# Kernel optimization log

Hardware: AMD Instinct MI355X
Metric: run time of the kernel (lower is better)

Reference implementation:

```python
import jax, jax.numpy as jnp
import numpy as np

ENT_TYPES = 9
INNER_DIM = 64
BIG_NEG = 1e12


def _rope_tables(seq_len, dim, dtype):
    # sinusoidal_position_embedding: interleaved [sin, cos] of pos * 10000^(-2i/d)
    pos = jnp.arange(seq_len, dtype=jnp.float32)[:, None]            # [S,1]
    inv_freq = jnp.power(10000.0, -2.0 * jnp.arange(dim // 2, dtype=jnp.float32) / dim)
    ang = pos * inv_freq                                             # [S,D/2]
    emb = jnp.stack([jnp.sin(ang), jnp.cos(ang)], axis=-1).reshape(seq_len, dim)  # [S,D]
    cos_pos = jnp.repeat(emb[:, 1::2], 2, axis=-1).astype(dtype)     # [S,D]
    sin_pos = jnp.repeat(emb[:, ::2], 2, axis=-1).astype(dtype)      # [S,D]
    return cos_pos, sin_pos


def _rotate_half(x):
    # stack([-x[...,1::2], x[...,::2]], -1).reshape(x.shape)
    return jnp.stack([-x[..., 1::2], x[..., ::2]], axis=-1).reshape(x.shape)


def setup_inputs() -> dict:
    key = jax.random.key(0)
    k1, k2 = jax.random.split(key)
    B, S, H = 16, 512, 1024
    last_hidden_state = jax.random.normal(k1, (B, S, H), dtype=jnp.float32)
    padding_mask = jnp.ones((B, S), dtype=jnp.float32)
    W = jax.random.normal(k2, (H, ENT_TYPES * INNER_DIM * 2), dtype=jnp.float32) * (1.0 / np.sqrt(H))
    b = jnp.zeros((ENT_TYPES * INNER_DIM * 2,), dtype=jnp.float32)
    return {"last_hidden_state": last_hidden_state, "padding_mask": padding_mask, "W": W, "b": b}


def reference(last_hidden_state, padding_mask, W, b):
    B, S, _ = last_hidden_state.shape
    H, D = ENT_TYPES, INNER_DIM
    out = last_hidden_state @ W + b                 # [B,S,H*2D]
    out = out.reshape(B, S, H, 2 * D)
    qw, kw = out[..., :D], out[..., D:]             # [B,S,H,D]

    cos_pos, sin_pos = _rope_tables(S, D, qw.dtype)  # [S,D]
    cos_pos = cos_pos[None, :, None, :]
    sin_pos = sin_pos[None, :, None, :]
    qw = qw * cos_pos + _rotate_half(qw) * sin_pos
    kw = kw * cos_pos + _rotate_half(kw) * sin_pos

    logits = jnp.einsum('bmhd,bnhd->bhmn', qw, kw)   # [B,H,S,S]
    pad = padding_mask[:, None, None, :]             # mask over key dim
    logits = logits * pad - (1.0 - pad) * BIG_NEG
    tril = jnp.tril(jnp.ones((S, S), dtype=logits.dtype), -1)
    logits = logits - tril * BIG_NEG
    return logits / jnp.sqrt(jnp.asarray(D, dtype=logits.dtype))
```

## Files before the change

kernel.cpp:

```cpp
#include <hip/hip_runtime.h>

#define EN 9
#define DD 64
#define SS 512
#define HH 1024
#define NOUT 1152

typedef float f32x4 __attribute__((ext_vector_type(4)));

#define GPTR(p) ((const __attribute__((address_space(1))) void*)(p))
#define LPTR(p) ((__attribute__((address_space(3))) void*)(p))

__device__ inline int pk4_fp8(float a, float b, float c, float d) {
  int v = __builtin_amdgcn_cvt_pk_fp8_f32(a, b, 0, false);
  v = __builtin_amdgcn_cvt_pk_fp8_f32(c, d, v, true);
  return v;
}

__global__ __launch_bounds__(256) void prep_kernel(
    const float* __restrict__ W, const float* __restrict__ X,
    unsigned char* __restrict__ Wf8, unsigned char* __restrict__ Xf8,
    float* __restrict__ ctab, float* __restrict__ stab) {
  if (blockIdx.x < 288u) {
    __shared__ float t[64][65];
    const int k0 = (blockIdx.x / 18) * 64;
    const int n0 = (blockIdx.x % 18) * 64;
    const int r = threadIdx.x >> 6;
    const int c = threadIdx.x & 63;
#pragma unroll
    for (int i = 0; i < 16; ++i) {
      const int kk = (i << 2) + r;
      t[kk][c] = W[(size_t)(k0 + kk) * NOUT + n0 + c];
    }
    __syncthreads();
#pragma unroll
    for (int i = 0; i < 2; ++i) {
      const int p = (i << 8) + threadIdx.x;
      const int n = p >> 3, cc = p & 7;
      const int kk = cc << 3;
      const int lo = pk4_fp8(t[kk][n], t[kk + 1][n], t[kk + 2][n], t[kk + 3][n]);
      const int hi =
          pk4_fp8(t[kk + 4][n], t[kk + 5][n], t[kk + 6][n], t[kk + 7][n]);
      const int gn = n0 + n;
      int2 v;
      v.x = lo;
      v.y = hi;
      *(int2*)(Wf8 + ((size_t)(k0 >> 6) * NOUT + gn) * 64 +
               ((cc ^ (gn & 7)) << 3)) = v;
    }
  } else if (blockIdx.x < 304u) {
    const int bt = blockIdx.x - 288;
#pragma unroll
    for (int j = 0; j < 4; ++j) {
      const int id = bt * 1024 + j * 256 + threadIdx.x;
      const int s = id >> 5, i = id & 31;
      const float freq = expf(-(float)(2 * i) * (9.210340371976184f / 64.0f));
      const float ang = (float)s * freq;
      ctab[id] = cosf(ang);
      stab[id] = sinf(ang);
    }
  } else {
    const int bt = blockIdx.x - 304;
#pragma unroll
    for (int j = 0; j < 4; ++j) {
      const int C = bt * 1024 + (j << 8) + threadIdx.x;
      const int row = C >> 7, c = C & 127;
      const float4 v0 = *(const float4*)(X + (size_t)C * 8);
      const float4 v1 = *(const float4*)(X + (size_t)C * 8 + 4);
      int2 v;
      v.x = pk4_fp8(v0.x, v0.y, v0.z, v0.w);
      v.y = pk4_fp8(v1.x, v1.y, v1.z, v1.w);
      *(int2*)(Xf8 + ((size_t)(c >> 3) * 8192 + row) * 64 +
               (((c ^ row) & 7) << 3)) = v;
    }
  }
}

__global__ __launch_bounds__(256, 4) void proj_rope_kernel(
    const unsigned char* __restrict__ Xf8, const unsigned char* __restrict__ Wf8,
    const float* __restrict__ bias, const float* __restrict__ ctab,
    const float* __restrict__ stab, unsigned char* __restrict__ QK) {
  __shared__ __align__(16) unsigned char sm[32768];
  const int tid = threadIdx.x;
  const int lane = tid & 63;
  const int wid = tid >> 6;
  const int wr = wid >> 1, wc = wid & 1;
  const int f = blockIdx.x;
  const int wkr = (f & 7) * 72 + (f >> 3);
  const int m0 = (wkr / 9) << 7;
  const int n0 = (wkr % 9) << 7;

  f32x4 acc[4][4];
#pragma unroll
  for (int i = 0; i < 4; ++i)
#pragma unroll
    for (int j = 0; j < 4; ++j) acc[i][j] = (f32x4){0.f, 0.f, 0.f, 0.f};

#define STAGE(BUF, T)                                                        \
  {                                                                          \
    const unsigned char* srcA_ = Xf8 + (((size_t)(T)*8192 + m0) << 6);       \
    const unsigned char* srcB_ = Wf8 + (((size_t)(T)*NOUT + n0) << 6);       \
    unsigned char* dst_ = sm + (BUF)*16384;                                  \
    _Pragma("unroll") for (int it = 0; it < 2; ++it) {                       \
      const int off_ = ((it << 8) + tid) << 4;                               \
      const int ldo_ = (((it << 8) + (wid << 6)) << 4);                      \
      __builtin_amdgcn_global_load_lds(GPTR(srcA_ + off_), LPTR(dst_ + ldo_), \
                                       16, 0, 0);                            \
      __builtin_amdgcn_global_load_lds(GPTR(srcB_ + off_),                   \
                                       LPTR(dst_ + 8192 + ldo_), 16, 0, 0);  \
    }                                                                        \
  }

#define COMPUTE(BUF)                                                         \
  {                                                                          \
    const unsigned char* smc_ = sm + (BUF)*16384;                            \
    __builtin_amdgcn_s_setprio(1);                                           \
    _Pragma("unroll") for (int kb = 0; kb < 2; ++kb) {                       \
      long aL[4], bL[4];                                                     \
      const int c8 = (kb << 2) + (lane >> 4);                                \
      _Pragma("unroll") for (int i = 0; i < 4; ++i) {                        \
        const int ra = (wr << 6) + (i << 4) + (lane & 15);                   \
        aL[i] = *(const long*)(smc_ + (ra << 6) + (((c8 ^ ra) & 7) << 3));   \
        const int rb = (wc << 6) + (i << 4) + (lane & 15);                   \
        bL[i] = *(const long*)(smc_ + 8192 + (rb << 6) +                     \
                               (((c8 ^ rb) & 7) << 3));                      \
      }                                                                      \
      _Pragma("unroll") for (int mi = 0; mi < 4; ++mi)                       \
          _Pragma("unroll") for (int ni = 0; ni < 4; ++ni) acc[mi][ni] =     \
          __builtin_amdgcn_mfma_f32_16x16x32_fp8_fp8(aL[mi], bL[ni],         \
                                                     acc[mi][ni], 0, 0, 0);  \
    }                                                                        \
    __builtin_amdgcn_s_setprio(0);                                           \
  }

  STAGE(0, 0)
#pragma unroll 1
  for (int t = 0; t < 15; ++t) {
    STAGE((t + 1) & 1, t + 1)
    asm volatile("s_waitcnt vmcnt(4)" ::: "memory");
    __builtin_amdgcn_s_barrier();
    __builtin_amdgcn_sched_barrier(0);
    COMPUTE(t & 1)
    __builtin_amdgcn_sched_barrier(0);
    __builtin_amdgcn_s_barrier();
  }
  asm volatile("s_waitcnt vmcnt(0)" ::: "memory");
  __builtin_amdgcn_s_barrier();
  __builtin_amdgcn_sched_barrier(0);
  COMPUTE(1)

  __syncthreads();
  float* scr = (float*)sm;
  const int erow = tid >> 3;
  const int ec8 = (tid & 7) << 1;
#pragma unroll
  for (int mi = 0; mi < 4; ++mi) {
#pragma unroll
    for (int ni = 0; ni < 4; ++ni) {
      const int col = (wc << 6) + (ni << 4) + (lane & 15);
#pragma unroll
      for (int r = 0; r < 4; ++r) {
        const int row = (wr << 4) + ((lane >> 4) << 2) + r;
        scr[row * 132 + col] = acc[mi][ni][r];
      }
    }
    __syncthreads();
    const int m = m0 + ((erow >> 4) << 6) + (mi << 4) + (erow & 15);
    const int s = m & (SS - 1);
    const int bb = m >> 9;
#pragma unroll
    for (int sl = 0; sl < 2; ++sl) {
      const int c8 = ec8 + sl;
      const int ncol = c8 << 3;
      const int n = n0 + ncol;
      const int h = n >> 7;
      const int t = (n >> 6) & 1;
      const int d0 = n & 63;
      const float scale = (t == 0) ? 0.125f : 1.0f;
      const float4 va = *(const float4*)&scr[erow * 132 + ncol];
      const float4 vb = *(const float4*)&scr[erow * 132 + ncol + 4];
      const float4 bia = *(const float4*)&bias[n];
      const float4 bib = *(const float4*)&bias[n + 4];
      const float4 cs = *(const float4*)&ctab[(s << 5) + (d0 >> 1)];
      const float4 sn = *(const float4*)&stab[(s << 5) + (d0 >> 1)];
      const float e0 = va.x + bia.x, o0 = va.y + bia.y;
      const float e1 = va.z + bia.z, o1 = va.w + bia.w;
      const float e2 = vb.x + bib.x, o2 = vb.y + bib.y;
      const float e3 = vb.z + bib.z, o3 = vb.w + bib.w;
      int2 ov;
      ov.x = pk4_fp8((e0 * cs.x - o0 * sn.x) * scale,
                     (o0 * cs.x + e0 * sn.x) * scale,
                     (e1 * cs.y - o1 * sn.y) * scale,
                     (o1 * cs.y + e1 * sn.y) * scale);
      ov.y = pk4_fp8((e2 * cs.z - o2 * sn.z) * scale,
                     (o2 * cs.z + e2 * sn.z) * scale,
                     (e3 * cs.w - o3 * sn.w) * scale,
                     (o3 * cs.w + e3 * sn.w) * scale);
      const int cswz = (((d0 >> 3) ^ (s & 7)) << 3);
      *(int2*)(QK + (((size_t)(bb * EN + h) * 2 + t) * SS + s) * DD + cswz) =
          ov;
    }
    __syncthreads();
  }
}

__global__ __launch_bounds__(256, 4) void logits_kernel(
    const unsigned char* __restrict__ QK, const float* __restrict__ pmask,
    float* __restrict__ out) {
  __shared__ __align__(16) unsigned char sm[16384];
  const int tid = threadIdx.x;
  const int lane = tid & 63;
  const int wid = tid >> 6;
  const int wr = wid >> 1, wc = wid & 1;
  const int f = blockIdx.x;
  const int wkr = (f & 7) * 288 + (f >> 3);
  const int bh = wkr >> 4;
  const int bb = bh / EN;
  const int tm = (wkr >> 2) & 3, tn = wkr & 3;
  const int mq0 = tm << 7, nk0 = tn << 7;
  const unsigned char* Qb = QK + (size_t)bh * 2 * SS * DD;
  const unsigned char* Kb = Qb + SS * DD;

#pragma unroll
  for (int it = 0; it < 2; ++it) {
    const int u = (it << 8) + tid;
    const int r = u >> 2, g = u & 3;
    __builtin_amdgcn_global_load_lds(
        GPTR(Qb + (size_t)(mq0 + r) * DD + (g << 4)),
        LPTR(sm + (((it << 8) + (wid << 6)) << 4)), 16, 0, 0);
    __builtin_amdgcn_global_load_lds(
        GPTR(Kb + (size_t)(nk0 + r) * DD + (g << 4)),
        LPTR(sm + 8192 + (((it << 8) + (wid << 6)) << 4)), 16, 0, 0);
  }
  __syncthreads();

  f32x4 acc[4][4];
#pragma unroll
  for (int i = 0; i < 4; ++i)
#pragma unroll
    for (int j = 0; j < 4; ++j) acc[i][j] = (f32x4){0.f, 0.f, 0.f, 0.f};

#pragma unroll
  for (int kb = 0; kb < 2; ++kb) {
    long aL[4], bL[4];
    const int c8 = (kb << 2) + (lane >> 4);
#pragma unroll
    for (int i = 0; i < 4; ++i) {
      const int ra = (wr << 6) + (i << 4) + (lane & 15);
      aL[i] = *(const long*)(sm + (ra << 6) + (((c8 ^ ra) & 7) << 3));
      const int rb = (wc << 6) + (i << 4) + (lane & 15);
      bL[i] = *(const long*)(sm + 8192 + (rb << 6) + (((c8 ^ rb) & 7) << 3));
    }
#pragma unroll
    for (int mi = 0; mi < 4; ++mi)
#pragma unroll
      for (int ni = 0; ni < 4; ++ni)
        acc[mi][ni] = __builtin_amdgcn_mfma_f32_16x16x32_fp8_fp8(
            aL[mi], bL[ni], acc[mi][ni], 0, 0, 0);
  }

#pragma unroll
  for (int mi = 0; mi < 4; ++mi) {
#pragma unroll
    for (int ni = 0; ni < 4; ++ni) {
      const int n = nk0 + (wc << 6) + (ni << 4) + (lane & 15);
      const float pd = pmask[bb * SS + n];
      const float sub = (1.0f - pd) * 1.25e11f;
#pragma unroll
      for (int r = 0; r < 4; ++r) {
        const int m = mq0 + (wr << 6) + (mi << 4) + ((lane >> 4) << 2) + r;
        float v = acc[mi][ni][r] * pd - sub;
        if (m > n) v -= 1.25e11f;
        out[((size_t)bh * SS + m) * SS + n] = v;
      }
    }
  }
}

extern "C" void kernel_launch(void* const* d_in, const int* in_sizes, int n_in,
                              void* d_out, int out_size, void* d_ws,
                              size_t ws_size, hipStream_t stream) {
  const float* X = (const float*)d_in[0];
  const float* pm = (const float*)d_in[1];
  const float* W = (const float*)d_in[2];
  const float* bias = (const float*)d_in[3];
  float* out = (float*)d_out;
  unsigned char* ws = (unsigned char*)d_ws;
  unsigned char* QK = ws;
  unsigned char* Wf8 = ws + 9437184;
  float* ctab = (float*)(ws + 10616832);
  float* stab = (float*)(ws + 10682368);
  unsigned char* Xf8 = ws + 10747904;

  prep_kernel<<<dim3(1328), dim3(256), 0, stream>>>(W, X, Wf8, Xf8, ctab, stab);
  proj_rope_kernel<<<dim3(576), dim3(256), 0, stream>>>(Xf8, Wf8, bias, ctab,
                                                        stab, QK);
  logits_kernel<<<dim3(2304), dim3(256), 0, stream>>>(QK, pm, out);
}
```

Baseline: 62.23 us.

## Load GEMM fragments directly from global memory, bypassing LDS staging

Both the projection GEMM and the logits GEMM now read their FP8 MFMA fragments straight from global memory into registers instead of staging tiles in LDS through global_load_lds with a double-buffered pipeline and barriers. This removes the LDS traffic and the synchronisation. It also drops the occupancy hint from launch_bounds. Each wave now issues redundant 8-byte global loads, which rely on L1/L2 for reuse, and the explicit load/compute overlap is gone, leaving only unroll-by-2 for latency hiding.

```diff
diff --git a/kernel.cpp b/kernel.cpp
--- a/kernel.cpp
+++ b/kernel.cpp
@@ -7,9 +7,6 @@
 #define NOUT 1152
 
 typedef float f32x4 __attribute__((ext_vector_type(4)));
-
-#define GPTR(p) ((const __attribute__((address_space(1))) void*)(p))
-#define LPTR(p) ((__attribute__((address_space(3))) void*)(p))
 
 __device__ inline int pk4_fp8(float a, float b, float c, float d) {
   int v = __builtin_amdgcn_cvt_pk_fp8_f32(a, b, 0, false);
@@ -76,11 +73,11 @@
   }
 }
 
-__global__ __launch_bounds__(256, 4) void proj_rope_kernel(
+__global__ __launch_bounds__(256) void proj_rope_kernel(
     const unsigned char* __restrict__ Xf8, const unsigned char* __restrict__ Wf8,
     const float* __restrict__ bias, const float* __restrict__ ctab,
     const float* __restrict__ stab, unsigned char* __restrict__ QK) {
-  __shared__ __align__(16) unsigned char sm[32768];
+  __shared__ __align__(16) float scr[32 * 132];
   const int tid = threadIdx.x;
   const int lane = tid & 63;
   const int wid = tid >> 6;
@@ -96,61 +93,34 @@
 #pragma unroll
     for (int j = 0; j < 4; ++j) acc[i][j] = (f32x4){0.f, 0.f, 0.f, 0.f};
 
-#define STAGE(BUF, T)                                                        \
-  {                                                                          \
-    const unsigned char* srcA_ = Xf8 + (((size_t)(T)*8192 + m0) << 6);       \
-    const unsigned char* srcB_ = Wf8 + (((size_t)(T)*NOUT + n0) << 6);       \
-    unsigned char* dst_ = sm + (BUF)*16384;                                  \
-    _Pragma("unroll") for (int it = 0; it < 2; ++it) {                       \
-      const int off_ = ((it << 8) + tid) << 4;                               \
-      const int ldo_ = (((it << 8) + (wid << 6)) << 4);                      \
-      __builtin_amdgcn_global_load_lds(GPTR(srcA_ + off_), LPTR(dst_ + ldo_), \
-                                       16, 0, 0);                            \
-      __builtin_amdgcn_global_load_lds(GPTR(srcB_ + off_),                   \
-                                       LPTR(dst_ + 8192 + ldo_), 16, 0, 0);  \
-    }                                                                        \
-  }
-
-#define COMPUTE(BUF)                                                         \
-  {                                                                          \
-    const unsigned char* smc_ = sm + (BUF)*16384;                            \
-    __builtin_amdgcn_s_setprio(1);                                           \
-    _Pragma("unroll") for (int kb = 0; kb < 2; ++kb) {                       \
-      long aL[4], bL[4];                                                     \
-      const int c8 = (kb << 2) + (lane >> 4);                                \
-      _Pragma("unroll") for (int i = 0; i < 4; ++i) {                        \
-        const int ra = (wr << 6) + (i << 4) + (lane & 15);                   \
-        aL[i] = *(const long*)(smc_ + (ra << 6) + (((c8 ^ ra) & 7) << 3));   \
-        const int rb = (wc << 6) + (i << 4) + (lane & 15);                   \
-        bL[i] = *(const long*)(smc_ + 8192 + (rb << 6) +                     \
-                               (((c8 ^ rb) & 7) << 3));                      \
-      }                                                                      \
-      _Pragma("unroll") for (int mi = 0; mi < 4; ++mi)                       \
-          _Pragma("unroll") for (int ni = 0; ni < 4; ++ni) acc[mi][ni] =     \
-          __builtin_amdgcn_mfma_f32_16x16x32_fp8_fp8(aL[mi], bL[ni],         \
-                                                     acc[mi][ni], 0, 0, 0);  \
-    }                                                                        \
-    __builtin_amdgcn_s_setprio(0);                                           \
-  }
-
-  STAGE(0, 0)
-#pragma unroll 1
-  for (int t = 0; t < 15; ++t) {
-    STAGE((t + 1) & 1, t + 1)
-    asm volatile("s_waitcnt vmcnt(4)" ::: "memory");
-    __builtin_amdgcn_s_barrier();
-    __builtin_amdgcn_sched_barrier(0);
-    COMPUTE(t & 1)
-    __builtin_amdgcn_sched_barrier(0);
-    __builtin_amdgcn_s_barrier();
-  }
-  asm volatile("s_waitcnt vmcnt(0)" ::: "memory");
-  __builtin_amdgcn_s_barrier();
-  __builtin_amdgcn_sched_barrier(0);
-  COMPUTE(1)
-
-  __syncthreads();
-  float* scr = (float*)sm;
+#pragma unroll 2
+  for (int T = 0; T < 16; ++T) {
+    const unsigned char* pa = Xf8 + (((size_t)T * 8192 + m0) << 6);
+    const unsigned char* pb = Wf8 + (((size_t)T * NOUT + n0) << 6);
+    long aL[2][4], bL[2][4];
+#pragma unroll
+    for (int kb = 0; kb < 2; ++kb) {
+      const int c8 = (kb << 2) + (lane >> 4);
+#pragma unroll
+      for (int i = 0; i < 4; ++i) {
+        const int ra = (wr << 6) + (i << 4) + (lane & 15);
+        aL[kb][i] = *(const long*)(pa + (ra << 6) + (((c8 ^ ra) & 7) << 3));
+        const int rb = (wc << 6) + (i << 4) + (lane & 15);
+        bL[kb][i] = *(const long*)(pb + (rb << 6) + (((c8 ^ rb) & 7) << 3));
+      }
+    }
+    __builtin_amdgcn_s_setprio(1);
+#pragma unroll
+    for (int kb = 0; kb < 2; ++kb)
+#pragma unroll
+      for (int mi = 0; mi < 4; ++mi)
+#pragma unroll
+        for (int ni = 0; ni < 4; ++ni)
+          acc[mi][ni] = __builtin_amdgcn_mfma_f32_16x16x32_fp8_fp8(
+              aL[kb][mi], bL[kb][ni], acc[mi][ni], 0, 0, 0);
+    __builtin_amdgcn_s_setprio(0);
+  }
+
   const int erow = tid >> 3;
   const int ec8 = (tid & 7) << 1;
 #pragma unroll
@@ -204,10 +174,9 @@
   }
 }
 
-__global__ __launch_bounds__(256, 4) void logits_kernel(
+__global__ __launch_bounds__(256) void logits_kernel(
     const unsigned char* __restrict__ QK, const float* __restrict__ pmask,
     float* __restrict__ out) {
-  __shared__ __align__(16) unsigned char sm[16384];
   const int tid = threadIdx.x;
   const int lane = tid & 63;
   const int wid = tid >> 6;
@@ -221,43 +190,34 @@
   const unsigned char* Qb = QK + (size_t)bh * 2 * SS * DD;
   const unsigned char* Kb = Qb + SS * DD;
 
-#pragma unroll
-  for (int it = 0; it < 2; ++it) {
-    const int u = (it << 8) + tid;
-    const int r = u >> 2, g = u & 3;
-    __builtin_amdgcn_global_load_lds(
-        GPTR(Qb + (size_t)(mq0 + r) * DD + (g << 4)),
-        LPTR(sm + (((it << 8) + (wid << 6)) << 4)), 16, 0, 0);
-    __builtin_amdgcn_global_load_lds(
-        GPTR(Kb + (size_t)(nk0 + r) * DD + (g << 4)),
-        LPTR(sm + 8192 + (((it << 8) + (wid << 6)) << 4)), 16, 0, 0);
-  }
-  __syncthreads();
-
   f32x4 acc[4][4];
 #pragma unroll
   for (int i = 0; i < 4; ++i)
 #pragma unroll
     for (int j = 0; j < 4; ++j) acc[i][j] = (f32x4){0.f, 0.f, 0.f, 0.f};
 
+  long aL[2][4], bL[2][4];
 #pragma unroll
   for (int kb = 0; kb < 2; ++kb) {
-    long aL[4], bL[4];
     const int c8 = (kb << 2) + (lane >> 4);
 #pragma unroll
     for (int i = 0; i < 4; ++i) {
       const int ra = (wr << 6) + (i << 4) + (lane & 15);
-      aL[i] = *(const long*)(sm + (ra << 6) + (((c8 ^ ra) & 7) << 3));
+      aL[kb][i] =
+          *(const long*)(Qb + ((size_t)(mq0 + ra) << 6) + (((c8 ^ ra) & 7) << 3));
       const int rb = (wc << 6) + (i << 4) + (lane & 15);
-      bL[i] = *(const long*)(sm + 8192 + (rb << 6) + (((c8 ^ rb) & 7) << 3));
-    }
+      bL[kb][i] =
+          *(const long*)(Kb + ((size_t)(nk0 + rb) << 6) + (((c8 ^ rb) & 7) << 3));
+    }
+  }
+#pragma unroll
+  for (int kb = 0; kb < 2; ++kb)
 #pragma unroll
     for (int mi = 0; mi < 4; ++mi)
 #pragma unroll
       for (int ni = 0; ni < 4; ++ni)
         acc[mi][ni] = __builtin_amdgcn_mfma_f32_16x16x32_fp8_fp8(
-            aL[mi], bL[ni], acc[mi][ni], 0, 0, 0);
-  }
+            aL[kb][mi], bL[kb][ni], acc[mi][ni], 0, 0, 0);
 
 #pragma unroll
   for (int mi = 0; mi < 4; ++mi) {
```

New measurement: 72.22 us. 16.0% more time.

## Halve projection GEMM M-tile to 64 rows and double block count

Applied to the files above, without the earlier changes.

The projection GEMM tile shrinks from 128x128 to 64x128, so 1152 blocks launch instead of 576. The warp layout becomes one row of four warps, each covering 32 columns, with fewer accumulators, smaller shared memory and a higher occupancy hint. The staging wait count and the epilogue indexing are adjusted to match. This aims to fill the 256 CUs better than 576 blocks did, at the cost of lower arithmetic intensity and more reloading of the W tile.

```diff
diff --git a/kernel.cpp b/kernel.cpp
--- a/kernel.cpp
+++ b/kernel.cpp
@@ -76,57 +76,58 @@
   }
 }
 
-__global__ __launch_bounds__(256, 4) void proj_rope_kernel(
+__global__ __launch_bounds__(256, 6) void proj_rope_kernel(
     const unsigned char* __restrict__ Xf8, const unsigned char* __restrict__ Wf8,
     const float* __restrict__ bias, const float* __restrict__ ctab,
     const float* __restrict__ stab, unsigned char* __restrict__ QK) {
-  __shared__ __align__(16) unsigned char sm[32768];
+  __shared__ __align__(16) unsigned char sm[24576];
   const int tid = threadIdx.x;
   const int lane = tid & 63;
   const int wid = tid >> 6;
-  const int wr = wid >> 1, wc = wid & 1;
   const int f = blockIdx.x;
-  const int wkr = (f & 7) * 72 + (f >> 3);
-  const int m0 = (wkr / 9) << 7;
+  const int wkr = (f & 7) * 144 + (f >> 3);
+  const int m0 = (wkr / 9) << 6;
   const int n0 = (wkr % 9) << 7;
 
-  f32x4 acc[4][4];
+  f32x4 acc[4][2];
 #pragma unroll
   for (int i = 0; i < 4; ++i)
 #pragma unroll
-    for (int j = 0; j < 4; ++j) acc[i][j] = (f32x4){0.f, 0.f, 0.f, 0.f};
+    for (int j = 0; j < 2; ++j) acc[i][j] = (f32x4){0.f, 0.f, 0.f, 0.f};
 
 #define STAGE(BUF, T)                                                        \
   {                                                                          \
     const unsigned char* srcA_ = Xf8 + (((size_t)(T)*8192 + m0) << 6);       \
     const unsigned char* srcB_ = Wf8 + (((size_t)(T)*NOUT + n0) << 6);       \
-    unsigned char* dst_ = sm + (BUF)*16384;                                  \
+    unsigned char* dstA_ = sm + (BUF)*4096;                                  \
+    unsigned char* dstB_ = sm + 8192 + (BUF)*8192;                           \
+    __builtin_amdgcn_global_load_lds(GPTR(srcA_ + (tid << 4)),               \
+                                     LPTR(dstA_ + (wid << 10)), 16, 0, 0);   \
     _Pragma("unroll") for (int it = 0; it < 2; ++it) {                       \
-      const int off_ = ((it << 8) + tid) << 4;                               \
-      const int ldo_ = (((it << 8) + (wid << 6)) << 4);                      \
-      __builtin_amdgcn_global_load_lds(GPTR(srcA_ + off_), LPTR(dst_ + ldo_), \
-                                       16, 0, 0);                            \
-      __builtin_amdgcn_global_load_lds(GPTR(srcB_ + off_),                   \
-                                       LPTR(dst_ + 8192 + ldo_), 16, 0, 0);  \
+      __builtin_amdgcn_global_load_lds(                                      \
+          GPTR(srcB_ + (((it << 8) + tid) << 4)),                            \
+          LPTR(dstB_ + (it << 12) + (wid << 10)), 16, 0, 0);                 \
     }                                                                        \
   }
 
 #define COMPUTE(BUF)                                                         \
   {                                                                          \
-    const unsigned char* smc_ = sm + (BUF)*16384;                            \
+    const unsigned char* smA_ = sm + (BUF)*4096;                             \
+    const unsigned char* smB_ = sm + 8192 + (BUF)*8192;                      \
     __builtin_amdgcn_s_setprio(1);                                           \
     _Pragma("unroll") for (int kb = 0; kb < 2; ++kb) {                       \
-      long aL[4], bL[4];                                                     \
+      long aL[4], bL[2];                                                     \
       const int c8 = (kb << 2) + (lane >> 4);                                \
       _Pragma("unroll") for (int i = 0; i < 4; ++i) {                        \
-        const int ra = (wr << 6) + (i << 4) + (lane & 15);                   \
-        aL[i] = *(const long*)(smc_ + (ra << 6) + (((c8 ^ ra) & 7) << 3));   \
-        const int rb = (wc << 6) + (i << 4) + (lane & 15);                   \
-        bL[i] = *(const long*)(smc_ + 8192 + (rb << 6) +                     \
-                               (((c8 ^ rb) & 7) << 3));                      \
+        const int ra = (i << 4) + (lane & 15);                               \
+        aL[i] = *(const long*)(smA_ + (ra << 6) + (((c8 ^ ra) & 7) << 3));   \
+      }                                                                      \
+      _Pragma("unroll") for (int j = 0; j < 2; ++j) {                        \
+        const int rb = (wid << 5) + (j << 4) + (lane & 15);                  \
+        bL[j] = *(const long*)(smB_ + (rb << 6) + (((c8 ^ rb) & 7) << 3));   \
       }                                                                      \
       _Pragma("unroll") for (int mi = 0; mi < 4; ++mi)                       \
-          _Pragma("unroll") for (int ni = 0; ni < 4; ++ni) acc[mi][ni] =     \
+          _Pragma("unroll") for (int ni = 0; ni < 2; ++ni) acc[mi][ni] =     \
           __builtin_amdgcn_mfma_f32_16x16x32_fp8_fp8(aL[mi], bL[ni],         \
                                                      acc[mi][ni], 0, 0, 0);  \
     }                                                                        \
@@ -137,7 +138,7 @@
 #pragma unroll 1
   for (int t = 0; t < 15; ++t) {
     STAGE((t + 1) & 1, t + 1)
-    asm volatile("s_waitcnt vmcnt(4)" ::: "memory");
+    asm volatile("s_waitcnt vmcnt(3)" ::: "memory");
     __builtin_amdgcn_s_barrier();
     __builtin_amdgcn_sched_barrier(0);
     COMPUTE(t & 1)
@@ -154,18 +155,22 @@
   const int erow = tid >> 3;
   const int ec8 = (tid & 7) << 1;
 #pragma unroll
-  for (int mi = 0; mi < 4; ++mi) {
-#pragma unroll
-    for (int ni = 0; ni < 4; ++ni) {
-      const int col = (wc << 6) + (ni << 4) + (lane & 15);
-#pragma unroll
-      for (int r = 0; r < 4; ++r) {
-        const int row = (wr << 4) + ((lane >> 4) << 2) + r;
-        scr[row * 132 + col] = acc[mi][ni][r];
+  for (int p = 0; p < 2; ++p) {
+#pragma unroll
+    for (int mh = 0; mh < 2; ++mh) {
+      const int mi = (p << 1) + mh;
+#pragma unroll
+      for (int ni = 0; ni < 2; ++ni) {
+        const int col = (wid << 5) + (ni << 4) + (lane & 15);
+#pragma unroll
+        for (int r = 0; r < 4; ++r) {
+          const int row = (mh << 4) + ((lane >> 4) << 2) + r;
+          scr[row * 132 + col] = acc[mi][ni][r];
+        }
       }
     }
     __syncthreads();
-    const int m = m0 + ((erow >> 4) << 6) + (mi << 4) + (erow & 15);
+    const int m = m0 + (p << 5) + erow;
     const int s = m & (SS - 1);
     const int bb = m >> 9;
 #pragma unroll
@@ -293,7 +298,7 @@
   unsigned char* Xf8 = ws + 10747904;
 
   prep_kernel<<<dim3(1328), dim3(256), 0, stream>>>(W, X, Wf8, Xf8, ctab, stab);
-  proj_rope_kernel<<<dim3(576), dim3(256), 0, stream>>>(Xf8, Wf8, bias, ctab,
-                                                        stab, QK);
+  proj_rope_kernel<<<dim3(1152), dim3(256), 0, stream>>>(Xf8, Wf8, bias, ctab,
+                                                         stab, QK);
   logits_kernel<<<dim3(2304), dim3(256), 0, stream>>>(QK, pm, out);
 }
```

Result: no change. 62.34 us (+0.2%).
